# Performance work log

Measured on AMD Instinct MI355X. Metric: run time of the kernel, lower is better.

## Reference

```python
import jax, jax.numpy as jnp
import numpy as np
from jax import lax

V, E, H, SEQ = 50257, 512, 512, 2048
TAGS, START, STOP = 12, 10, 11
NEG = -10000.0


def _lstm_dir(x, Wih, Whh, bih, bhh, reverse):
    # x: [T, in], Wih: [4H, in], Whh: [4H, H] (torch gate order i,f,g,o)
    h0 = jnp.zeros((Whh.shape[1],), x.dtype)
    c0 = jnp.zeros((Whh.shape[1],), x.dtype)
    b = bih + bhh

    def step(carry, xt):
        h, c = carry
        gates = Wih @ xt + Whh @ h + b  # [4H]
        i, f, g, o = jnp.split(gates, 4)
        c = jax.nn.sigmoid(f) * c + jax.nn.sigmoid(i) * jnp.tanh(g)
        h = jax.nn.sigmoid(o) * jnp.tanh(c)
        return (h, c), h

    _, hs = lax.scan(step, (h0, c0), x, reverse=reverse)
    return hs  # [T, H]


def _bilstm_layer(x, Wih, Whh, bih, bhh):
    # stacked params: leading dim 2 = (fwd, bwd)
    fwd = _lstm_dir(x, Wih[0], Whh[0], bih[0], bhh[0], False)
    bwd = _lstm_dir(x, Wih[1], Whh[1], bih[1], bhh[1], True)
    return jnp.concatenate([fwd, bwd], axis=-1)  # [T, 2H]


def _viterbi(feats, transitions):
    # feats: [T, TAGS]; transitions[next, prev]
    init = jnp.full((TAGS,), NEG, feats.dtype).at[START].set(0.0)

    def step(fv, feat):
        scores = fv[None, :] + transitions  # [next, prev]
        bptr = jnp.argmax(scores, axis=1)
        fv_new = jnp.max(scores, axis=1) + feat
        return fv_new, bptr

    fv, bptrs = lax.scan(step, init, feats)
    terminal = fv + transitions[STOP]
    best_last = jnp.argmax(terminal)
    path_score = terminal[best_last]

    def back(tag, bp):
        prev = bp[tag]
        return prev, prev

    _, ys = lax.scan(back, best_last, bptrs, reverse=True)
    # ys[t] = path[t-1]; ys[0] = START (dropped); append best_last
    best_path = jnp.concatenate([ys[1:], best_last[None]])
    return path_score, best_path


def setup_inputs() -> dict:
    key = jax.random.key(0)
    ks = jax.random.split(key, 16)
    s = lambda *sh: 1.0 / np.sqrt(H)
    inp = {
        "sentence": jax.random.randint(ks[0], (SEQ,), 0, V),
        "emb": jax.random.normal(ks[1], (V, E), jnp.float32),
        "Wih0": jax.random.uniform(ks[2], (2, 4 * H, E), jnp.float32, -s(), s()),
        "Whh0": jax.random.uniform(ks[3], (2, 4 * H, H), jnp.float32, -s(), s()),
        "bih0": jax.random.uniform(ks[4], (2, 4 * H), jnp.float32, -s(), s()),
        "bhh0": jax.random.uniform(ks[5], (2, 4 * H), jnp.float32, -s(), s()),
        "Wih1": jax.random.uniform(ks[6], (2, 4 * H, 2 * H), jnp.float32, -s(), s()),
        "Whh1": jax.random.uniform(ks[7], (2, 4 * H, H), jnp.float32, -s(), s()),
        "bih1": jax.random.uniform(ks[8], (2, 4 * H), jnp.float32, -s(), s()),
        "bhh1": jax.random.uniform(ks[9], (2, 4 * H), jnp.float32, -s(), s()),
        "W_tag": jax.random.uniform(ks[10], (TAGS, 2 * H), jnp.float32, -0.1, 0.1),
        "b_tag": jnp.zeros((TAGS,), jnp.float32),
    }
    trans = jax.random.normal(ks[11], (TAGS, TAGS), jnp.float32)
    trans = trans.at[START, :].set(NEG).at[:, STOP].set(NEG)
    inp["transitions"] = trans
    return inp


def reference(sentence, emb, Wih0, Whh0, bih0, bhh0, Wih1, Whh1, bih1, bhh1, W_tag, b_tag, transitions):
    x = emb[sentence]  # [T, E]  (dropout identity in eval)
    x = _bilstm_layer(x, Wih0, Whh0, bih0, bhh0)
    x = _bilstm_layer(x, Wih1, Whh1, bih1, bhh1)
    feats = x @ W_tag.T + b_tag  # [T, TAGS]
    path_score, best_path = _viterbi(feats, transitions)
    return path_score, best_path
```

## Files before the change

kernel.cpp:

```cpp
#include <hip/hip_runtime.h>
#include <math.h>

#define SEQ 2048
#define EMB_D 512
#define HID 512
#define NTAGS 12
#define START_TAG 10
#define STOP_TAG 11
#define NEGV (-10000.0f)
#define POISON 0xAAAAAAAAu

__device__ __forceinline__ float sigf(float x) { return 1.0f / (1.0f + expf(-x)); }

__global__ void k_embed(const int* __restrict__ sent, const float* __restrict__ emb,
                        float* __restrict__ x0) {
    int t = blockIdx.x;
    int tid = threadIdx.x;
    int row = sent[t];
    const float4* src = (const float4*)(emb + (size_t)row * EMB_D);
    float4* dst = (float4*)(x0 + (size_t)t * EMB_D);
    dst[tid] = src[tid];
}

#define BM 64
#define BN 64
#define BKT 32
#define LDT 68

__global__ __launch_bounds__(256) void k_gemm(
    const float* __restrict__ Af, const float* __restrict__ Ab,
    const float* __restrict__ B,
    const float* __restrict__ biasA, const float* __restrict__ biasB,
    float* __restrict__ C, int K) {
    const int N = 2048;
    int dir = blockIdx.z;
    const float* Bd = B + (size_t)dir * N * K;
    const float* bA = biasA + dir * N;
    const float* bB = biasB + dir * N;
    float* Cd = C + (size_t)dir * 2048 * N;
    int m0 = blockIdx.y * BM, n0 = blockIdx.x * BN;

    __shared__ float As[BKT * LDT];
    __shared__ float Bs[BKT * LDT];

    int tid = threadIdx.x;
    int lrow = tid >> 2;
    int lk4 = (tid & 3) * 8;
    int tx = tid & 15, ty = tid >> 4;

    float acc[4][4] = {};

    for (int kt = 0; kt < K; kt += BKT) {
        {
            int m = m0 + lrow;
#pragma unroll
            for (int hh = 0; hh < 2; ++hh) {
                int k = kt + lk4 + hh * 4;
                const float* src = (k < 512) ? (Af + (size_t)m * 512 + k)
                                             : (Ab + (size_t)m * 512 + (k - 512));
                float4 v = *(const float4*)src;
                int kl = lk4 + hh * 4;
                As[(kl + 0) * LDT + lrow] = v.x;
                As[(kl + 1) * LDT + lrow] = v.y;
                As[(kl + 2) * LDT + lrow] = v.z;
                As[(kl + 3) * LDT + lrow] = v.w;
            }
        }
        {
            int n = n0 + lrow;
#pragma unroll
            for (int hh = 0; hh < 2; ++hh) {
                int k = kt + lk4 + hh * 4;
                float4 v = *(const float4*)(Bd + (size_t)n * K + k);
                int kl = lk4 + hh * 4;
                Bs[(kl + 0) * LDT + lrow] = v.x;
                Bs[(kl + 1) * LDT + lrow] = v.y;
                Bs[(kl + 2) * LDT + lrow] = v.z;
                Bs[(kl + 3) * LDT + lrow] = v.w;
            }
        }
        __syncthreads();
#pragma unroll
        for (int kk = 0; kk < BKT; ++kk) {
            float4 av = *(const float4*)&As[kk * LDT + ty * 4];
            float4 bv = *(const float4*)&Bs[kk * LDT + tx * 4];
            acc[0][0] += av.x * bv.x; acc[0][1] += av.x * bv.y; acc[0][2] += av.x * bv.z; acc[0][3] += av.x * bv.w;
            acc[1][0] += av.y * bv.x; acc[1][1] += av.y * bv.y; acc[1][2] += av.y * bv.z; acc[1][3] += av.y * bv.w;
            acc[2][0] += av.z * bv.x; acc[2][1] += av.z * bv.y; acc[2][2] += av.z * bv.z; acc[2][3] += av.z * bv.w;
            acc[3][0] += av.w * bv.x; acc[3][1] += av.w * bv.y; acc[3][2] += av.w * bv.z; acc[3][3] += av.w * bv.w;
        }
        __syncthreads();
    }
#pragma unroll
    for (int i = 0; i < 4; ++i) {
        int m = m0 + ty * 4 + i;
#pragma unroll
        for (int j = 0; j < 4; ++j) {
            int n = n0 + tx * 4 + j;
            Cd[(size_t)m * N + n] = acc[i][j] + bA[n] + bB[n];
        }
    }
}

#define HPAD 132

__global__ __launch_bounds__(256, 1) void k_lstm(
    const float* __restrict__ Whh,
    const float* __restrict__ Gi,
    float* __restrict__ hstore)
{
    int wg = blockIdx.x;
    int dir = wg >> 5;
    int slice = wg & 31;
    int u_base = slice * 16;
    int tid = threadIdx.x;

    const float* Whh_d = Whh + (size_t)dir * 2048 * 512;
    const float* Gi_d = Gi + (size_t)dir * 2048 * 2048;
    float* h_d = hstore + (size_t)dir * 2048 * 512;

    int rl = tid >> 2;
    int kp = tid & 3;
    int gg = rl >> 4;
    int uu = rl & 15;
    int r = gg * 512 + u_base + uu;

    float w[128];
    {
        const float* wsrc = Whh_d + (size_t)r * 512 + kp * 128;
#pragma unroll
        for (int j = 0; j < 128; j += 4) {
            float4 v = *(const float4*)(wsrc + j);
            w[j] = v.x; w[j + 1] = v.y; w[j + 2] = v.z; w[j + 3] = v.w;
        }
    }

    __shared__ __align__(16) float hlds[4 * HPAD];
    __shared__ float gdot[64];
    float c_reg = 0.0f;

    int sec = tid >> 6;
    int soff = (tid & 63) * 2;
    float* hstage = hlds + sec * HPAD + soff;

    for (int it = 0; it < 2048; ++it) {
        int t = dir ? (2047 - it) : it;

        float gi = 0.f;
        if (kp == 0) gi = Gi_d[(size_t)t * 2048 + r];

        if (it == 0) {
            hstage[0] = 0.f;
            hstage[1] = 0.f;
        } else {
            int tprev = dir ? (t + 1) : (t - 1);
            const unsigned long long* src =
                (const unsigned long long*)(h_d + (size_t)tprev * 512) + tid;
            unsigned long long v;
            do {
                v = __hip_atomic_load(src, __ATOMIC_RELAXED, __HIP_MEMORY_SCOPE_AGENT);
            } while ((unsigned)v == POISON || (unsigned)(v >> 32) == POISON);
            hstage[0] = __uint_as_float((unsigned)v);
            hstage[1] = __uint_as_float((unsigned)(v >> 32));
        }
        __syncthreads();

        float p = 0.f;
        const float4* h4 = (const float4*)(hlds + kp * HPAD);
#pragma unroll
        for (int j4 = 0; j4 < 32; ++j4) {
            float4 hv = h4[j4];
            p += w[4 * j4 + 0] * hv.x;
            p += w[4 * j4 + 1] * hv.y;
            p += w[4 * j4 + 2] * hv.z;
            p += w[4 * j4 + 3] * hv.w;
        }
        p += __shfl_xor(p, 1);
        p += __shfl_xor(p, 2);
        if (kp == 0) {
            float v = p + gi;
            gdot[rl] = (gg == 2) ? tanhf(v) : sigf(v);
        }
        __syncthreads();

        if (tid < 16) {
            float iv = gdot[0 * 16 + tid];
            float fv = gdot[1 * 16 + tid];
            float gv = gdot[2 * 16 + tid];
            float ov = gdot[3 * 16 + tid];
            float c = fv * c_reg + iv * gv;
            float h = ov * tanhf(c);
            c_reg = c;
            __hip_atomic_store(h_d + (size_t)t * 512 + u_base + tid, h,
                               __ATOMIC_RELAXED, __HIP_MEMORY_SCOPE_AGENT);
        }
    }
}

__global__ __launch_bounds__(64) void k_feats(
    const float* __restrict__ h1,
    const float* __restrict__ Wt,
    const float* __restrict__ bt,
    float* __restrict__ feats)
{
    int t = blockIdx.x;
    int lane = threadIdx.x;
    __shared__ __align__(16) float xl[1024];
    const float4* hf = (const float4*)(h1 + (size_t)t * 512);
    const float4* hb = (const float4*)(h1 + (size_t)(2048 + t) * 512);
    ((float4*)xl)[lane] = hf[lane];
    ((float4*)xl)[lane + 64] = hf[lane + 64];
    ((float4*)xl)[128 + lane] = hb[lane];
    ((float4*)xl)[128 + lane + 64] = hb[lane + 64];
    __syncthreads();
    for (int tag = 0; tag < NTAGS; ++tag) {
        const float* wrow = Wt + tag * 1024;
        float s = 0.f;
        for (int k = lane; k < 1024; k += 64) s += xl[k] * wrow[k];
#pragma unroll
        for (int off = 32; off; off >>= 1) s += __shfl_xor(s, off);
        if (lane == 0) feats[t * NTAGS + tag] = s + bt[tag];
    }
}

__global__ __launch_bounds__(64) void k_viterbi(
    const float* __restrict__ feats, const float* __restrict__ trans,
    float* __restrict__ out) {
    __shared__ float fv[2][NTAGS];
    __shared__ unsigned char bp[SEQ * NTAGS];
    __shared__ float featbuf[256 * NTAGS];
    __shared__ float term[NTAGS];
    int lane = threadIdx.x;

    float tr[NTAGS];
    if (lane < NTAGS) {
#pragma unroll
        for (int p = 0; p < NTAGS; ++p) tr[p] = trans[lane * NTAGS + p];
        fv[0][lane] = (lane == START_TAG) ? 0.f : NEGV;
    }
    __syncthreads();

    int cur = 0;
    for (int tc = 0; tc < SEQ; tc += 256) {
        for (int i = lane; i < 256 * NTAGS; i += 64) featbuf[i] = feats[tc * NTAGS + i];
        __syncthreads();
        for (int tt = 0; tt < 256; ++tt) {
            int t = tc + tt;
            if (lane < NTAGS) {
                float best = fv[cur][0] + tr[0];
                int bi = 0;
#pragma unroll
                for (int p = 1; p < NTAGS; ++p) {
                    float s = fv[cur][p] + tr[p];
                    if (s > best) { best = s; bi = p; }
                }
                bp[t * NTAGS + lane] = (unsigned char)bi;
                fv[cur ^ 1][lane] = best + featbuf[tt * NTAGS + lane];
            }
            cur ^= 1;
            __syncthreads();
        }
    }

    if (lane < NTAGS) term[lane] = fv[cur][lane] + trans[STOP_TAG * NTAGS + lane];
    __syncthreads();
    if (lane == 0) {
        float best = term[0];
        int bi = 0;
        for (int p = 1; p < NTAGS; ++p) {
            if (term[p] > best) { best = term[p]; bi = p; }
        }
        out[0] = best;
        int tag = bi;
        out[1 + (SEQ - 1)] = (float)tag;
        for (int t = SEQ - 1; t >= 1; --t) {
            tag = bp[t * NTAGS + tag];
            out[t] = (float)tag;
        }
    }
}

extern "C" void kernel_launch(void* const* d_in, const int* in_sizes, int n_in,
                              void* d_out, int out_size, void* d_ws, size_t ws_size,
                              hipStream_t stream) {
    const int* sent = (const int*)d_in[0];
    const float* emb = (const float*)d_in[1];
    const float* Wih0 = (const float*)d_in[2];
    const float* Whh0 = (const float*)d_in[3];
    const float* bih0 = (const float*)d_in[4];
    const float* bhh0 = (const float*)d_in[5];
    const float* Wih1 = (const float*)d_in[6];
    const float* Whh1 = (const float*)d_in[7];
    const float* bih1 = (const float*)d_in[8];
    const float* bhh1 = (const float*)d_in[9];
    const float* Wtag = (const float*)d_in[10];
    const float* btag = (const float*)d_in[11];
    const float* trans = (const float*)d_in[12];
    float* out = (float*)d_out;

    char* ws = (char*)d_ws;
    size_t off = 0;
    auto alloc = [&](size_t bytes) {
        void* p = ws + off;
        off += (bytes + 255) & ~(size_t)255;
        return p;
    };
    float* x0 = (float*)alloc(2048ull * 512 * 4);
    float* Gi = (float*)alloc(2ull * 2048 * 2048 * 4);
    float* h0 = (float*)alloc(2ull * 2048 * 512 * 4);
    float* h1 = (float*)alloc(2ull * 2048 * 512 * 4);
    float* feats = (float*)alloc(2048ull * NTAGS * 4);

    hipMemsetAsync(h0, 0xAA, 2ull * 2048 * 512 * 4, stream);
    hipMemsetAsync(h1, 0xAA, 2ull * 2048 * 512 * 4, stream);

    k_embed<<<2048, 128, 0, stream>>>(sent, emb, x0);

    dim3 gg(32, 32, 2);
    k_gemm<<<gg, 256, 0, stream>>>(x0, x0, Wih0, bih0, bhh0, Gi, 512);
    k_lstm<<<64, 256, 0, stream>>>(Whh0, Gi, h0);
    k_gemm<<<gg, 256, 0, stream>>>(h0, h0 + 2048ull * 512, Wih1, bih1, bhh1, Gi, 1024);
    k_lstm<<<64, 256, 0, stream>>>(Whh1, Gi, h1);
    k_feats<<<2048, 64, 0, stream>>>(h1, Wtag, btag, feats);
    k_viterbi<<<1, 64, 0, stream>>>(feats, trans, out);
}
```

Before: 8.902 ms.

## Remap LSTM gate rows so the cell update uses shuffles, dropping one barrier

Rows are reassigned so the four gates of each hidden unit sit in the same wavefront. The cell and hidden update can then be done with cross-lane shuffles, which removes the gdot shared buffer and the second __syncthreads in every recurrent step. The input-projection value Gi for the next timestep is prefetched one step ahead, so its load latency overlaps the current step's dot product. Hidden outputs are written as packed 64-bit atomic stores, matching the 64-bit poll on the reader side. The gate math is now computed redundantly on all four k-partition lanes, and the indexing relies on a specific lane layout.

```diff
diff --git a/kernel.cpp b/kernel.cpp
--- a/kernel.cpp
+++ b/kernel.cpp
@@ -121,8 +121,8 @@
 
     int rl = tid >> 2;
     int kp = tid & 3;
-    int gg = rl >> 4;
-    int uu = rl & 15;
+    int uu = rl >> 2;
+    int gg = rl & 3;
     int r = gg * 512 + u_base + uu;
 
     float w[128];
@@ -136,18 +136,17 @@
     }
 
     __shared__ __align__(16) float hlds[4 * HPAD];
-    __shared__ float gdot[64];
     float c_reg = 0.0f;
 
     int sec = tid >> 6;
     int soff = (tid & 63) * 2;
     float* hstage = hlds + sec * HPAD + soff;
 
+    int t0 = dir ? 2047 : 0;
+    float gi = Gi_d[(size_t)t0 * 2048 + r];
+
     for (int it = 0; it < 2048; ++it) {
         int t = dir ? (2047 - it) : it;
-
-        float gi = 0.f;
-        if (kp == 0) gi = Gi_d[(size_t)t * 2048 + r];
 
         if (it == 0) {
             hstage[0] = 0.f;
@@ -165,6 +164,12 @@
         }
         __syncthreads();
 
+        float gi_next = 0.f;
+        if (it + 1 < 2048) {
+            int tn = dir ? (t - 1) : (t + 1);
+            gi_next = Gi_d[(size_t)tn * 2048 + r];
+        }
+
         float p = 0.f;
         const float4* h4 = (const float4*)(hlds + kp * HPAD);
 #pragma unroll
@@ -177,23 +182,31 @@
         }
         p += __shfl_xor(p, 1);
         p += __shfl_xor(p, 2);
-        if (kp == 0) {
-            float v = p + gi;
-            gdot[rl] = (gg == 2) ? tanhf(v) : sigf(v);
-        }
-        __syncthreads();
-
-        if (tid < 16) {
-            float iv = gdot[0 * 16 + tid];
-            float fv = gdot[1 * 16 + tid];
-            float gv = gdot[2 * 16 + tid];
-            float ov = gdot[3 * 16 + tid];
-            float c = fv * c_reg + iv * gv;
-            float h = ov * tanhf(c);
-            c_reg = c;
-            __hip_atomic_store(h_d + (size_t)t * 512 + u_base + tid, h,
-                               __ATOMIC_RELAXED, __HIP_MEMORY_SCOPE_AGENT);
-        }
+
+        float v = p + gi;
+        float a = (gg == 2) ? tanhf(v) : sigf(v);
+        float b = __shfl_xor(a, 8);
+        float term;
+        if (gg == 0 || gg == 2) term = a * b;
+        else if (gg == 1)       term = a * c_reg;
+        else                    term = b * c_reg;
+        float d = __shfl_xor(term, 4);
+        float c_new = term + d;
+        c_reg = c_new;
+
+        if (gg == 3) {
+            float hv = a * tanhf(c_new);
+            float hv2 = __shfl_xor(hv, 16);
+            if (kp == 0 && (uu & 1) == 0) {
+                unsigned long long pk =
+                    (unsigned long long)__float_as_uint(hv) |
+                    ((unsigned long long)__float_as_uint(hv2) << 32);
+                __hip_atomic_store(
+                    (unsigned long long*)(h_d + (size_t)t * 512 + u_base + uu),
+                    pk, __ATOMIC_RELAXED, __HIP_MEMORY_SCOPE_AGENT);
+            }
+        }
+        gi = gi_next;
     }
 }
 
```

After: 14.14 ms. 58.8% more time.
